# Kernel optimization log

Hardware: AMD Instinct MI355X
Metric: run time of the kernel (lower is better)

Reference implementation:

```python
import jax, jax.numpy as jnp
import numpy as np

B, T, V, E = 8, 256, 32000, 512
ENC_H, DEC_H, DEC_IN = 512, 512, 512
MAX_OOVS = 100


def setup_inputs() -> dict:
    key = jax.random.key(0)
    ks = jax.random.split(key, 7)
    output_logits = jax.random.normal(ks[0], (B, T, V), dtype=jnp.float32)
    attn_weights = jax.random.uniform(ks[1], (B, T, E), dtype=jnp.float32)
    decoder_hidden_state = jax.random.normal(ks[2], (B, T, 2 * DEC_H), dtype=jnp.float32)
    decoder_input = jax.random.normal(ks[3], (B, T, DEC_IN), dtype=jnp.float32)
    context_vector = jax.random.normal(ks[4], (B, T, ENC_H), dtype=jnp.float32)
    encoder_input = jax.random.randint(ks[5], (B, E), 0, V + MAX_OOVS, dtype=jnp.int64)
    pgen_w = jax.random.normal(ks[6], (1, ENC_H + 2 * DEC_H + DEC_IN), dtype=jnp.float32) * 0.02
    pgen_b = jnp.zeros((1,), dtype=jnp.float32)
    return {
        "output_logits": output_logits,
        "attn_weights": attn_weights,
        "decoder_hidden_state": decoder_hidden_state,
        "decoder_input": decoder_input,
        "context_vector": context_vector,
        "encoder_input": encoder_input,
        "pgen_w": pgen_w,
        "pgen_b": pgen_b,
        "max_oovs": MAX_OOVS,
    }


def reference(output_logits, attn_weights, decoder_hidden_state, decoder_input,
              context_vector, encoder_input, pgen_w, pgen_b, max_oovs):
    b, t, v = output_logits.shape
    # softmax over vocab, then zero-pad to extended vocab [b, t, v + max_oovs]
    probs = jax.nn.softmax(output_logits, axis=-1)
    probs_ext = jnp.pad(probs, ((0, 0), (0, 0), (0, max_oovs)))
    # pgen = sigmoid(Linear([context; dec_hidden; dec_input]))  -> [b, t, 1]
    pre = jnp.concatenate([context_vector, decoder_hidden_state, decoder_input], axis=-1)
    pgen = jax.nn.sigmoid(jnp.einsum('btf,of->bto', pre, pgen_w) + pgen_b)
    pcopy = 1.0 - pgen
    # scatter_add attention weights into extended-vocab copy distribution
    bi = jnp.arange(b)[:, None, None]           # [b,1,1]
    ti = jnp.arange(t)[None, :, None]           # [1,t,1]
    idx = encoder_input[:, None, :]             # [b,1,E] broadcast over t
    copy_probs = jnp.zeros_like(probs_ext).at[bi, ti, idx].add(attn_weights)
    total = pgen * probs_ext + pcopy * copy_probs
    return (total, pgen)
```

## Files before the change

### kernel.cpp

```cpp
#include <hip/hip_runtime.h>
#include <cmath>

#define B_    8
#define T_    256
#define V_    32000
#define E_    512
#define OOV_  100
#define VE_   (V_ + OOV_)
#define ROWS_ (B_ * T_)
#define NV4_  (V_ / 4)
#define TAIL_ (NV4_ - 7 * 1024)
#define PAD4_ (OOV_ / 4)
#define TOTAL_ ((size_t)ROWS_ * VE_)

__global__ __launch_bounds__(1024) void pg_fused_kernel(
    const float* __restrict__ logits,
    const float* __restrict__ attn,
    const float* __restrict__ ctx,
    const float* __restrict__ hid,
    const float* __restrict__ dec,
    const int*   __restrict__ enc,
    const float* __restrict__ pw,
    const float* __restrict__ pb,
    float* __restrict__ out_total,
    float* __restrict__ out_pgen)
{
  const int row  = blockIdx.x;
  const int tid  = threadIdx.x;
  const int lane = tid & 63;
  const int wid  = tid >> 6;
  __shared__ float redA[16];
  __shared__ float redB[16];

  float att_v = 0.f;
  int   att_i = 0;
  if (tid < E_) {
    att_v = attn[row * E_ + tid];
    att_i = enc[((row >> 8) << 9) + tid];
  }

  float acc = 0.f;
  #pragma unroll
  for (int k = 0; k < 2; ++k) {
    const int f = tid + (k << 10);
    float pv;
    if (f < 512)       pv = ctx[row * 512 + f];
    else if (f < 1536) pv = hid[row * 1024 + (f - 512)];
    else               pv = dec[row * 512 + (f - 1536)];
    acc += pv * pw[f];
  }
  #pragma unroll
  for (int o = 32; o > 0; o >>= 1) acc += __shfl_xor(acc, o);
  if (lane == 0) redA[wid] = acc;
  __syncthreads();
  if (tid < 16) {
    float x = redA[tid];
    #pragma unroll
    for (int o = 8; o > 0; o >>= 1) x += __shfl_xor(x, o);
    if (tid == 0) redA[0] = x;
  }
  __syncthreads();
  const float pgen = 1.f / (1.f + __expf(-(redA[0] + pb[0])));
  __syncthreads();

  const float4* lrow = (const float4*)(logits + (size_t)row * V_);
  float m = -3.0e38f;
  float s = 0.f;
  #pragma unroll
  for (int k = 0; k < 7; ++k) {
    const float4 x = lrow[tid + (k << 10)];
    const float xm = fmaxf(fmaxf(x.x, x.y), fmaxf(x.z, x.w));
    const float nm = fmaxf(m, xm);
    const float e0 = __expf(x.x - nm), e1 = __expf(x.y - nm);
    const float e2 = __expf(x.z - nm), e3 = __expf(x.w - nm);
    s = s * __expf(m - nm) + ((e0 + e1) + (e2 + e3));
    m = nm;
  }
  if (tid < TAIL_) {
    const float4 x = lrow[tid + 7168];
    const float xm = fmaxf(fmaxf(x.x, x.y), fmaxf(x.z, x.w));
    const float nm = fmaxf(m, xm);
    const float e0 = __expf(x.x - nm), e1 = __expf(x.y - nm);
    const float e2 = __expf(x.z - nm), e3 = __expf(x.w - nm);
    s = s * __expf(m - nm) + ((e0 + e1) + (e2 + e3));
    m = nm;
  }

  #pragma unroll
  for (int o = 32; o > 0; o >>= 1) {
    const float om = __shfl_xor(m, o);
    const float os = __shfl_xor(s, o);
    const float nm = fmaxf(m, om);
    s = s * __expf(m - nm) + os * __expf(om - nm);
    m = nm;
  }
  if (lane == 0) { redA[wid] = m; redB[wid] = s; }
  __syncthreads();
  if (tid < 16) {
    float mm = redA[tid], ss = redB[tid];
    #pragma unroll
    for (int o = 8; o > 0; o >>= 1) {
      const float om = __shfl_xor(mm, o);
      const float os = __shfl_xor(ss, o);
      const float nm = fmaxf(mm, om);
      ss = ss * __expf(mm - nm) + os * __expf(om - nm);
      mm = nm;
    }
    if (tid == 0) { redA[0] = mm; redB[0] = ss; }
  }
  __syncthreads();
  const float M = redA[0];
  const float scale = pgen / redB[0];

  float4* orow = (float4*)(out_total + (size_t)row * VE_);
  #pragma unroll
  for (int k = 0; k < 7; ++k) {
    const int i = tid + (k << 10);
    const float4 x = lrow[i];
    float4 y;
    y.x = scale * __expf(x.x - M);
    y.y = scale * __expf(x.y - M);
    y.z = scale * __expf(x.z - M);
    y.w = scale * __expf(x.w - M);
    orow[i] = y;
  }
  if (tid < TAIL_) {
    const float4 x = lrow[tid + 7168];
    float4 y;
    y.x = scale * __expf(x.x - M);
    y.y = scale * __expf(x.y - M);
    y.z = scale * __expf(x.z - M);
    y.w = scale * __expf(x.w - M);
    orow[tid + 7168] = y;
  }
  if (tid < PAD4_) orow[NV4_ + tid] = make_float4(0.f, 0.f, 0.f, 0.f);
  if (tid == 0) out_pgen[row] = pgen;

  __syncthreads();
  if (tid < E_) {
    unsafeAtomicAdd(out_total + (size_t)row * VE_ + att_i,
                    (1.f - pgen) * att_v);
  }
}

extern "C" void kernel_launch(void* const* d_in, const int* in_sizes, int n_in,
                              void* d_out, int out_size, void* d_ws, size_t ws_size,
                              hipStream_t stream) {
  const float* logits = (const float*)d_in[0];
  const float* attn   = (const float*)d_in[1];
  const float* hid    = (const float*)d_in[2];
  const float* dec    = (const float*)d_in[3];
  const float* ctx    = (const float*)d_in[4];
  const int*   enc    = (const int*)d_in[5];
  const float* pw     = (const float*)d_in[6];
  const float* pb     = (const float*)d_in[7];

  float* out_total = (float*)d_out;
  float* out_pgen  = out_total + TOTAL_;

  pg_fused_kernel<<<ROWS_, 1024, 0, stream>>>(
      logits, attn, ctx, hid, dec, enc, pw, pb, out_total, out_pgen);
}
```

Before: 497.8 us.

## Shrink blocks to 256 threads with multiple online-softmax accumulators per thread

The block size drops from 1024 to 256 threads per row, so each thread now processes 31+ float4 chunks instead of 7, and launch bounds ask for 8 blocks per CU. The online max/sum uses four independent accumulators to break the dependency chain. The second-level reductions become simple serial loops over 4 warp partials, which removes a barrier. The goal is better occupancy and latency hiding for this memory-bound softmax. The cost is more serial work per thread and more register pressure.

```diff
diff --git a/kernel.cpp b/kernel.cpp
--- a/kernel.cpp
+++ b/kernel.cpp
@@ -1,19 +1,20 @@
 #include <hip/hip_runtime.h>
 #include <cmath>
 
-#define B_    8
-#define T_    256
-#define V_    32000
-#define E_    512
-#define OOV_  100
-#define VE_   (V_ + OOV_)
-#define ROWS_ (B_ * T_)
-#define NV4_  (V_ / 4)
-#define TAIL_ (NV4_ - 7 * 1024)
-#define PAD4_ (OOV_ / 4)
+#define B_     8
+#define T_     256
+#define V_     32000
+#define E_     512
+#define OOV_   100
+#define VE_    (V_ + OOV_)
+#define ROWS_  (B_ * T_)
+#define NV4_   (V_ / 4)
+#define KFULL_ 31
+#define TAILT_ (NV4_ - KFULL_ * 256)
+#define PAD4_  (OOV_ / 4)
 #define TOTAL_ ((size_t)ROWS_ * VE_)
 
-__global__ __launch_bounds__(1024) void pg_fused_kernel(
+__global__ __launch_bounds__(256, 8) void pg_fused_kernel(
     const float* __restrict__ logits,
     const float* __restrict__ attn,
     const float* __restrict__ ctx,
@@ -29,20 +30,19 @@
   const int tid  = threadIdx.x;
   const int lane = tid & 63;
   const int wid  = tid >> 6;
-  __shared__ float redA[16];
-  __shared__ float redB[16];
+  __shared__ float redA[4];
+  __shared__ float redB[4];
 
-  float att_v = 0.f;
-  int   att_i = 0;
-  if (tid < E_) {
-    att_v = attn[row * E_ + tid];
-    att_i = enc[((row >> 8) << 9) + tid];
-  }
+  const int b = row >> 8;
+  const float av0 = attn[row * E_ + tid];
+  const float av1 = attn[row * E_ + tid + 256];
+  const int   ai0 = enc[b * E_ + tid];
+  const int   ai1 = enc[b * E_ + tid + 256];
 
   float acc = 0.f;
   #pragma unroll
-  for (int k = 0; k < 2; ++k) {
-    const int f = tid + (k << 10);
+  for (int k = 0; k < 8; ++k) {
+    const int f = tid + (k << 8);
     float pv;
     if (f < 512)       pv = ctx[row * 512 + f];
     else if (f < 1536) pv = hid[row * 1024 + (f - 512)];
@@ -53,38 +53,39 @@
   for (int o = 32; o > 0; o >>= 1) acc += __shfl_xor(acc, o);
   if (lane == 0) redA[wid] = acc;
   __syncthreads();
-  if (tid < 16) {
-    float x = redA[tid];
-    #pragma unroll
-    for (int o = 8; o > 0; o >>= 1) x += __shfl_xor(x, o);
-    if (tid == 0) redA[0] = x;
+  float pgen;
+  {
+    const float dot = redA[0] + redA[1] + redA[2] + redA[3];
+    pgen = 1.f / (1.f + __expf(-(dot + pb[0])));
   }
-  __syncthreads();
-  const float pgen = 1.f / (1.f + __expf(-(redA[0] + pb[0])));
   __syncthreads();
 
   const float4* lrow = (const float4*)(logits + (size_t)row * V_);
-  float m = -3.0e38f;
-  float s = 0.f;
-  #pragma unroll
-  for (int k = 0; k < 7; ++k) {
-    const float4 x = lrow[tid + (k << 10)];
+  float mm[4] = {-3.0e38f, -3.0e38f, -3.0e38f, -3.0e38f};
+  float ss[4] = {0.f, 0.f, 0.f, 0.f};
+  #pragma unroll 8
+  for (int k = 0; k < KFULL_; ++k) {
+    const int j = k & 3;
+    const float4 x = lrow[tid + (k << 8)];
     const float xm = fmaxf(fmaxf(x.x, x.y), fmaxf(x.z, x.w));
-    const float nm = fmaxf(m, xm);
+    const float nm = fmaxf(mm[j], xm);
     const float e0 = __expf(x.x - nm), e1 = __expf(x.y - nm);
     const float e2 = __expf(x.z - nm), e3 = __expf(x.w - nm);
-    s = s * __expf(m - nm) + ((e0 + e1) + (e2 + e3));
-    m = nm;
+    ss[j] = ss[j] * __expf(mm[j] - nm) + ((e0 + e1) + (e2 + e3));
+    mm[j] = nm;
   }
-  if (tid < TAIL_) {
-    const float4 x = lrow[tid + 7168];
+  if (tid < TAILT_) {
+    const float4 x = lrow[KFULL_ * 256 + tid];
     const float xm = fmaxf(fmaxf(x.x, x.y), fmaxf(x.z, x.w));
-    const float nm = fmaxf(m, xm);
+    const float nm = fmaxf(mm[0], xm);
     const float e0 = __expf(x.x - nm), e1 = __expf(x.y - nm);
     const float e2 = __expf(x.z - nm), e3 = __expf(x.w - nm);
-    s = s * __expf(m - nm) + ((e0 + e1) + (e2 + e3));
-    m = nm;
+    ss[0] = ss[0] * __expf(mm[0] - nm) + ((e0 + e1) + (e2 + e3));
+    mm[0] = nm;
   }
+  float m = fmaxf(fmaxf(mm[0], mm[1]), fmaxf(mm[2], mm[3]));
+  float s = ss[0] * __expf(mm[0] - m) + ss[1] * __expf(mm[1] - m)
+          + ss[2] * __expf(mm[2] - m) + ss[3] * __expf(mm[3] - m);
 
   #pragma unroll
   for (int o = 32; o > 0; o >>= 1) {
@@ -96,26 +97,20 @@
   }
   if (lane == 0) { redA[wid] = m; redB[wid] = s; }
   __syncthreads();
-  if (tid < 16) {
-    float mm = redA[tid], ss = redB[tid];
-    #pragma unroll
-    for (int o = 8; o > 0; o >>= 1) {
-      const float om = __shfl_xor(mm, o);
-      const float os = __shfl_xor(ss, o);
-      const float nm = fmaxf(mm, om);
-      ss = ss * __expf(mm - nm) + os * __expf(om - nm);
-      mm = nm;
-    }
-    if (tid == 0) { redA[0] = mm; redB[0] = ss; }
+  float M = redA[0], S = redB[0];
+  #pragma unroll
+  for (int w = 1; w < 4; ++w) {
+    const float om = redA[w], os = redB[w];
+    const float nm = fmaxf(M, om);
+    S = S * __expf(M - nm) + os * __expf(om - nm);
+    M = nm;
   }
-  __syncthreads();
-  const float M = redA[0];
-  const float scale = pgen / redB[0];
+  const float scale = pgen / S;
 
   float4* orow = (float4*)(out_total + (size_t)row * VE_);
-  #pragma unroll
-  for (int k = 0; k < 7; ++k) {
-    const int i = tid + (k << 10);
+  #pragma unroll 8
+  for (int k = 0; k < KFULL_; ++k) {
+    const int i = tid + (k << 8);
     const float4 x = lrow[i];
     float4 y;
     y.x = scale * __expf(x.x - M);
@@ -124,23 +119,24 @@
     y.w = scale * __expf(x.w - M);
     orow[i] = y;
   }
-  if (tid < TAIL_) {
-    const float4 x = lrow[tid + 7168];
+  if (tid < TAILT_) {
+    const int i = KFULL_ * 256 + tid;
+    const float4 x = lrow[i];
     float4 y;
     y.x = scale * __expf(x.x - M);
     y.y = scale * __expf(x.y - M);
     y.z = scale * __expf(x.z - M);
     y.w = scale * __expf(x.w - M);
-    orow[tid + 7168] = y;
+    orow[i] = y;
   }
   if (tid < PAD4_) orow[NV4_ + tid] = make_float4(0.f, 0.f, 0.f, 0.f);
   if (tid == 0) out_pgen[row] = pgen;
 
   __syncthreads();
-  if (tid < E_) {
-    unsafeAtomicAdd(out_total + (size_t)row * VE_ + att_i,
-                    (1.f - pgen) * att_v);
-  }
+  const float pc = 1.f - pgen;
+  float* rbase = out_total + (size_t)row * VE_;
+  unsafeAtomicAdd(rbase + ai0, pc * av0);
+  unsafeAtomicAdd(rbase + ai1, pc * av1);
 }
 
 extern "C" void kernel_launch(void* const* d_in, const int* in_sizes, int n_in,
@@ -158,6 +154,6 @@
   float* out_total = (float*)d_out;
   float* out_pgen  = out_total + TOTAL_;
 
-  pg_fused_kernel<<<ROWS_, 1024, 0, stream>>>(
+  pg_fused_kernel<<<ROWS_, 256, 0, stream>>>(
       logits, attn, ctx, hid, dec, enc, pw, pb, out_total, out_pgen);
 }
```

New measurement: 519.8 us. +4.4%, slower.
